# Optimization experiments

Hardware: AMD Instinct MI355X
Metric: run time of the kernel (lower is better)

The kernel has to match this reference:

```python
import jax, jax.numpy as jnp
import numpy as np

BETA = 0.25  # VectorQuantizer commitment beta


def setup_inputs() -> dict:
    key = jax.random.key(0)
    k1, k2, k3, k4 = jax.random.split(key, 4)
    B, T, Zc, D, K = 8, 4096, 512, 256, 8192
    x = jax.random.normal(k1, (B, T, 1, Zc), dtype=jnp.float32)
    W = jax.random.normal(k2, (Zc, D), dtype=jnp.float32) / np.sqrt(Zc)
    b = jax.random.normal(k3, (D,), dtype=jnp.float32) * 0.01
    codebook = jax.random.normal(k4, (K, D), dtype=jnp.float32) / np.sqrt(D)
    return {"x": x, "W": W, "b": b, "codebook": codebook}


def reference(x, W, b, codebook):
    sg = jax.lax.stop_gradient
    # quant_conv: Linear(z_channels -> embed_dim) after squeezing dim 2
    h = jnp.einsum('btc,cd->btd', jnp.squeeze(x, 2), W) + b  # [B,T,D]
    B, T, D = h.shape
    flat = h.reshape(-1, D)  # [B*T, D]
    # squared L2 distances to codebook: ||z||^2 + ||e||^2 - 2 z.e
    d = (jnp.sum(flat * flat, axis=1, keepdims=True)
         + jnp.sum(codebook * codebook, axis=1)
         - 2.0 * flat @ codebook.T)  # [B*T, K]
    idx = jnp.argmin(d, axis=1)  # [B*T]
    zq = jnp.take(codebook, idx, axis=0).reshape(B, T, D)
    # codebook + commitment loss
    emb_loss = (BETA * jnp.mean((sg(zq) - h) ** 2)
                + jnp.mean((zq - sg(h)) ** 2))
    # straight-through estimator
    zq = h + sg(zq - h)
    quant = zq[..., None]  # [B,T,D,1], matching h.unsqueeze(-1) layout
    return quant, emb_loss
```

## Files before the change

kernel.cpp:

```cpp
#include <hip/hip_runtime.h>
#include <stdint.h>

#define M_TOT 32768
#define ZC 512
#define DD 256
#define KCODES 8192
#define NGRAN 512
#define MARGIN 0.15f
#define NBUCKET 256

typedef _Float16 half8   __attribute__((ext_vector_type(8)));
typedef _Float16 half2v  __attribute__((ext_vector_type(2)));
typedef float    float4v __attribute__((ext_vector_type(4)));
typedef float    float16v __attribute__((ext_vector_type(16)));

#define OFF_H     0ull
#define OFF_HT    33554432ull
#define OFF_CBT   50331648ull
#define OFF_HH    54525952ull
#define OFF_EE    54657024ull
#define OFF_LOSSP 54689792ull
#define OFF_SMIN  54691840ull
#define OFF_WTH   OFF_SMIN
#define OFF_WTL   (OFF_SMIN + 524288ull)

#define ASYNC_CP16(gp, lp)                                                     \
  __builtin_amdgcn_global_load_lds(                                            \
      (const __attribute__((address_space(1))) void*)(gp),                     \
      (__attribute__((address_space(3))) void*)(lp), 16, 0, 0)

__global__ __launch_bounds__(256) void k_prep_w(const float* __restrict__ W,
                                                _Float16* __restrict__ wt_hi,
                                                _Float16* __restrict__ wt_lo) {
    const int idx = blockIdx.x * 256 + threadIdx.x;
    const int n = idx & 255, k = idx >> 8;
    const float v = W[(size_t)k * DD + n];
    const _Float16 hi = (_Float16)v;
    const _Float16 lo = (_Float16)(v - (float)hi);
    const int off = (((n >> 5) * 64 + (k >> 3)) << 8) + ((n & 31) << 3) + (k & 7);
    wt_hi[off] = hi;
    wt_lo[off] = lo;
}

__global__ __launch_bounds__(256) void k_gemm1(const float* __restrict__ x,
                                               const _Float16* __restrict__ wt_hi,
                                               const _Float16* __restrict__ wt_lo,
                                               const float* __restrict__ b,
                                               float* __restrict__ h) {
    __shared__ _Float16 sH[64 * 64];
    __shared__ _Float16 sL[64 * 64];
    const int tid = threadIdx.x, lane = tid & 63, w = tid >> 6;
    const int wy = w >> 1, wx = w & 1;
    const int m0 = blockIdx.x * 64;

    float16v acc[4];
#pragma unroll
    for (int j = 0; j < 4; ++j) acc[j] = (float16v)(0.0f);

    for (int kb = 0; kb < ZC; kb += 64) {
        __syncthreads();
        {
            const int m = tid & 63;
            const int kp = tid >> 6;
#pragma unroll
            for (int i2 = 0; i2 < 2; ++i2) {
                const int kg = kp * 2 + i2;
                const float* src = x + (size_t)(m0 + m) * ZC + kb + kg * 8;
                float4v v0 = *(const float4v*)src;
                float4v v1 = *(const float4v*)(src + 4);
                half8 hi, lo;
                float vv[8] = {v0.x, v0.y, v0.z, v0.w, v1.x, v1.y, v1.z, v1.w};
#pragma unroll
                for (int j = 0; j < 8; ++j) {
                    hi[j] = (_Float16)vv[j];
                    lo[j] = (_Float16)(vv[j] - (float)hi[j]);
                }
                const int off = (((m >> 5) * 8 + kg) << 8) + ((m & 31) << 3);
                *(half8*)&sH[off] = hi;
                *(half8*)&sL[off] = lo;
            }
        }
        __syncthreads();
#pragma unroll
        for (int s = 0; s < 4; ++s) {
            const int S = (kb >> 4) + s;
            half8 ah = *(const half8*)&sH[((wy * 8 + 2 * s) << 8) + lane * 8];
            half8 al = *(const half8*)&sL[((wy * 8 + 2 * s) << 8) + lane * 8];
#pragma unroll
            for (int nf = 0; nf < 4; ++nf) {
                const int nblk = wx * 4 + nf;
                const size_t boff = ((size_t)(nblk * 64 + 2 * S) << 8) + lane * 8;
                half8 bh = *(const half8*)&wt_hi[boff];
                half8 bl = *(const half8*)&wt_lo[boff];
                acc[nf] = __builtin_amdgcn_mfma_f32_32x32x16_f16(ah, bh, acc[nf], 0, 0, 0);
                acc[nf] = __builtin_amdgcn_mfma_f32_32x32x16_f16(ah, bl, acc[nf], 0, 0, 0);
                acc[nf] = __builtin_amdgcn_mfma_f32_32x32x16_f16(al, bh, acc[nf], 0, 0, 0);
            }
        }
    }
#pragma unroll
    for (int nf = 0; nf < 4; ++nf) {
        const int col = wx * 128 + nf * 32 + (lane & 31);
        const float bias = b[col];
#pragma unroll
        for (int r = 0; r < 16; ++r) {
            const int row = m0 + wy * 32 + (r & 3) + 8 * (r >> 2) + 4 * (lane >> 5);
            h[(size_t)row * DD + col] = acc[nf][r] + bias;
        }
    }
}

__global__ __launch_bounds__(256) void k_prep_h(const float* __restrict__ h,
                                                _Float16* __restrict__ ht,
                                                float* __restrict__ hh) {
    const int lane = threadIdx.x & 63, w = threadIdx.x >> 6;
    const int row = blockIdx.x * 4 + w;
    float4v v = *(const float4v*)&h[(size_t)row * DD + lane * 4];
    half2v p0, p1;
    p0.x = (_Float16)v.x; p0.y = (_Float16)v.y;
    p1.x = (_Float16)v.z; p1.y = (_Float16)v.w;
    const size_t off = ((size_t)((row >> 5) * 32 + (lane >> 1)) << 8) +
                       ((row & 31) << 3) + ((lane & 1) << 2);
    *(half2v*)&ht[off] = p0;
    *(half2v*)&ht[off + 2] = p1;
    float s = v.x * v.x + v.y * v.y + v.z * v.z + v.w * v.w;
#pragma unroll
    for (int o = 32; o; o >>= 1) s += __shfl_down(s, o);
    if (lane == 0) hh[row] = s;
}

__global__ __launch_bounds__(256) void k_prep_cb(const float* __restrict__ cb,
                                                 _Float16* __restrict__ cbt,
                                                 float* __restrict__ ee,
                                                 float* __restrict__ loss_part) {
    if (blockIdx.x == 0) loss_part[threadIdx.x] = 0.0f;
    const int lane = threadIdx.x & 63, w = threadIdx.x >> 6;
    const int code = blockIdx.x * 4 + w;
    float4v v = *(const float4v*)&cb[(size_t)code * DD + lane * 4];
    half2v p0, p1;
    p0.x = (_Float16)v.x; p0.y = (_Float16)v.y;
    p1.x = (_Float16)v.z; p1.y = (_Float16)v.w;
    const size_t off = ((size_t)((code >> 5) * 32 + (lane >> 1)) << 8) +
                       ((code & 31) << 3) + ((lane & 1) << 2);
    *(half2v*)&cbt[off] = p0;
    *(half2v*)&cbt[off + 2] = p1;
    float s = v.x * v.x + v.y * v.y + v.z * v.z + v.w * v.w;
#pragma unroll
    for (int o = 32; o; o >>= 1) s += __shfl_down(s, o);
    if (lane == 0) ee[code] = s;
}

__global__ __launch_bounds__(256, 2) void k_dist(const _Float16* __restrict__ ht,
                                                 const _Float16* __restrict__ cbt,
                                                 const float* __restrict__ ee,
                                                 _Float16* __restrict__ smin) {
    __shared__ _Float16 sB[2][64 * 256];
    const int tid = threadIdx.x, lane = tid & 63, w = tid >> 6;
    const int lw = lane & 31, csel = lane >> 5;
    const int bx = blockIdx.x;
    const int by = blockIdx.y;

    half8 afr[2][16];
    const size_t lo = (size_t)lane * 8;
#pragma unroll
    for (int mi = 0; mi < 2; ++mi) {
        const _Float16* base = cbt + (size_t)(bx * 8 + w * 2 + mi) * 8192;
#pragma unroll
        for (int s = 0; s < 16; ++s)
            afr[mi][s] = *(const half8*)(base + s * 512 + lo);
    }
    half8 aext[2], bext;
#pragma unroll
    for (int j = 0; j < 8; ++j) bext[j] = (_Float16)0.f;
    if (csel == 0) bext[0] = (_Float16)(-0.5f);
#pragma unroll
    for (int mi = 0; mi < 2; ++mi) {
        const float e = ee[bx * 256 + w * 64 + mi * 32 + lw];
#pragma unroll
        for (int j = 0; j < 8; ++j) aext[mi][j] = (_Float16)0.f;
        if (csel == 0) aext[mi][0] = (_Float16)e;
    }

    const _Float16* hbase = ht + (size_t)by * 1024 * 256 + (size_t)w * 4096 + lane * 8;
#define STAGE_HS(buf, t)                                                       \
    do {                                                                       \
        const _Float16* g_ = hbase + (size_t)(t) * 16384;                      \
        char* l_ = (char*)&sB[(buf)][0] + w * 8192;                            \
        _Pragma("unroll")                                                      \
        for (int i_ = 0; i_ < 8; ++i_)                                         \
            ASYNC_CP16(g_ + i_ * 512, l_ + i_ * 1024);                         \
    } while (0)

#define COMPUTE_HS(buf, t)                                                     \
    do {                                                                       \
        const int r0_ = by * 1024 + (t) * 64;                                  \
        const _Float16* sb_ = &sB[(buf)][0];                                   \
        _Pragma("unroll 1")                                                    \
        for (int nj = 0; nj < 2; ++nj) {                                       \
            float16v acc0 = (float16v)(0.f), acc1 = (float16v)(0.f);           \
            __builtin_amdgcn_s_setprio(1);                                     \
            _Pragma("unroll")                                                  \
            for (int s = 0; s < 16; ++s) {                                     \
                half8 bf = *(const half8*)&sb_[(size_t)((nj * 32 + 2 * s + csel) << 8) + lw * 8]; \
                acc0 = __builtin_amdgcn_mfma_f32_32x32x16_f16(afr[0][s], bf, acc0, 0, 0, 0); \
                acc1 = __builtin_amdgcn_mfma_f32_32x32x16_f16(afr[1][s], bf, acc1, 0, 0, 0); \
            }                                                                  \
            acc0 = __builtin_amdgcn_mfma_f32_32x32x16_f16(aext[0], bext, acc0, 0, 0, 0); \
            acc1 = __builtin_amdgcn_mfma_f32_32x32x16_f16(aext[1], bext, acc1, 0, 0, 0); \
            __builtin_amdgcn_s_setprio(0);                                     \
             \
             \
            float g0a = acc0[0], g1a = acc0[8];                                \
            float g0b = acc1[0], g1b = acc1[8];                                \
            _Pragma("unroll")                                                  \
            for (int r = 1; r < 8; ++r) {                                      \
                g0a = fmaxf(g0a, acc0[r]);  g1a = fmaxf(g1a, acc0[8 + r]);     \
                g0b = fmaxf(g0b, acc1[r]);  g1b = fmaxf(g1b, acc1[8 + r]);     \
            }                                                                  \
            g0a = fmaxf(g0a, __shfl_xor(g0a, 32));                             \
            g1a = fmaxf(g1a, __shfl_xor(g1a, 32));                             \
            g0b = fmaxf(g0b, __shfl_xor(g0b, 32));                             \
            g1b = fmaxf(g1b, __shfl_xor(g1b, 32));                             \
            if (lane < 32) {                                                   \
                const int row_ = r0_ + nj * 32 + lane;                         \
                const int gb_ = bx * 16 + w * 4;                               \
                smin[(size_t)(gb_ + 0) * M_TOT + row_] = (_Float16)(-2.f * g0a); \
                smin[(size_t)(gb_ + 1) * M_TOT + row_] = (_Float16)(-2.f * g1a); \
                smin[(size_t)(gb_ + 2) * M_TOT + row_] = (_Float16)(-2.f * g0b); \
                smin[(size_t)(gb_ + 3) * M_TOT + row_] = (_Float16)(-2.f * g1b); \
            }                                                                  \
        }                                                                      \
    } while (0)

    STAGE_HS(0, 0);

#pragma unroll 1
    for (int t = 0; t < 15; ++t) {
        const int cur = t & 1;
        STAGE_HS(cur ^ 1, t + 1);
        asm volatile("s_waitcnt vmcnt(8)" ::: "memory");
        __builtin_amdgcn_s_barrier();
        __builtin_amdgcn_sched_barrier(0);
        COMPUTE_HS(cur, t);
        __builtin_amdgcn_sched_barrier(0);
        __builtin_amdgcn_s_barrier();
    }
    asm volatile("s_waitcnt vmcnt(0)" ::: "memory");
    __builtin_amdgcn_s_barrier();
    __builtin_amdgcn_sched_barrier(0);
    COMPUTE_HS(1, 15);

#undef STAGE_HS
#undef COMPUTE_HS
}

__global__ __launch_bounds__(256, 2) void k_select(const float* __restrict__ h,
                                                   const float* __restrict__ cb,
                                                   const float* __restrict__ hh,
                                                   const float* __restrict__ ee,
                                                   const _Float16* __restrict__ smin,
                                                   float* __restrict__ out,
                                                   float* __restrict__ loss_part) {
    __shared__ _Float16 sS[64][512];
    const int t = threadIdx.x, lane = t & 63, w = t >> 6;
    const int r0 = blockIdx.x * 64;

    for (int gi = t; gi < NGRAN; gi += 256) {
        const _Float16* src = smin + (size_t)gi * M_TOT + r0;
#pragma unroll
        for (int c = 0; c < 8; ++c) {
            half8 v = *(const half8*)(src + c * 8);
#pragma unroll
            for (int j = 0; j < 8; ++j) sS[c * 8 + j][gi] = v[j];
        }
    }
    __syncthreads();

    float lossacc = 0.0f;
    for (int i = 0; i < 16; ++i) {
        const int row = r0 + w * 16 + i;
        float4v hv = *(const float4v*)&h[(size_t)row * DD + lane * 4];
        half8 sm = *(const half8*)&sS[w * 16 + i][lane * 8];
        float vmin = 1e30f;
        float sv[8];
#pragma unroll
        for (int j = 0; j < 8; ++j) {
            sv[j] = (float)sm[j];
            vmin = fminf(vmin, sv[j]);
        }
        float m2 = vmin;
#pragma unroll
        for (int o = 32; o; o >>= 1) m2 = fminf(m2, __shfl_xor(m2, o));
        const float thr = m2 + MARGIN;
        unsigned flags = 0;
#pragma unroll
        for (int j = 0; j < 8; ++j)
            if (sv[j] <= thr) flags |= (1u << j);

        unsigned long long act = __ballot(flags != 0);
        unsigned long long bestk = ~0ull;
        const float hhv = hh[row];
        while (act) {
            const int ln = __ffsll((long long)act) - 1;
            act &= act - 1;
            unsigned fl = (unsigned)__shfl((int)flags, ln);
            while (fl) {
                const int j = __ffs(fl) - 1;
                fl &= fl - 1;
                const int g = ln * 8 + j;
#pragma unroll
                for (int c = 0; c < 16; ++c) {
                    const int code = g * 16 + c;
                    float4v cv = *(const float4v*)&cb[(size_t)code * DD + lane * 4];
                    float s = hv.x * cv.x + hv.y * cv.y + hv.z * cv.z + hv.w * cv.w;
#pragma unroll
                    for (int o = 32; o; o >>= 1) s += __shfl_xor(s, o);
                    const float d = (hhv + ee[code]) - 2.0f * s;
                    const unsigned bts = __float_as_uint(d);
                    const unsigned mb =
                        bts ^ (unsigned)(((int)bts >> 31) | 0x80000000);
                    const unsigned long long key =
                        ((unsigned long long)mb << 32) | (unsigned)code;
                    if (key < bestk) bestk = key;
                }
            }
        }
        const unsigned best = (unsigned)(bestk & 0xffffffffull);
        float4v cv = *(const float4v*)&cb[(size_t)best * DD + lane * 4];
        *(float4v*)&out[(size_t)row * DD + lane * 4] = cv;
        const float dx = cv.x - hv.x, dy = cv.y - hv.y;
        const float dz = cv.z - hv.z, dw = cv.w - hv.w;
        lossacc += dx * dx + dy * dy + dz * dz + dw * dw;
    }
#pragma unroll
    for (int o = 32; o; o >>= 1) lossacc += __shfl_xor(lossacc, o);
    if (lane == 0)
        atomicAdd(&loss_part[(blockIdx.x * 4 + w) & (NBUCKET - 1)], lossacc);
}

__global__ __launch_bounds__(256) void k_final(const float* __restrict__ loss_part,
                                               float* __restrict__ out) {
    const int t = threadIdx.x;
    float s = loss_part[t];
#pragma unroll
    for (int off = 32; off; off >>= 1) s += __shfl_down(s, off);
    __shared__ float wsum[4];
    if ((t & 63) == 0) wsum[t >> 6] = s;
    __syncthreads();
    if (t == 0)
        out[0] = 1.25f * ((wsum[0] + wsum[1]) + (wsum[2] + wsum[3]))
                 / (float)(M_TOT * DD);
}

extern "C" void kernel_launch(void* const* d_in, const int* in_sizes, int n_in,
                              void* d_out, int out_size, void* d_ws, size_t ws_size,
                              hipStream_t stream) {
    const float* x  = (const float*)d_in[0];
    const float* W  = (const float*)d_in[1];
    const float* b  = (const float*)d_in[2];
    const float* cb = (const float*)d_in[3];
    float* out = (float*)d_out;

    char* ws = (char*)d_ws;
    float* h        = (float*)(ws + OFF_H);
    _Float16* ht    = (_Float16*)(ws + OFF_HT);
    _Float16* cbt   = (_Float16*)(ws + OFF_CBT);
    _Float16* wt_hi = (_Float16*)(ws + OFF_WTH);
    _Float16* wt_lo = (_Float16*)(ws + OFF_WTL);
    float* hh       = (float*)(ws + OFF_HH);
    float* ee       = (float*)(ws + OFF_EE);
    _Float16* smin  = (_Float16*)(ws + OFF_SMIN);
    float* loss_part = (float*)(ws + OFF_LOSSP);

    hipLaunchKernelGGL(k_prep_w, dim3(512), dim3(256), 0, stream, W, wt_hi, wt_lo);
    hipLaunchKernelGGL(k_prep_cb, dim3(KCODES / 4), dim3(256), 0, stream,
                       cb, cbt, ee, loss_part);
    hipLaunchKernelGGL(k_gemm1, dim3(M_TOT / 64), dim3(256), 0, stream,
                       x, wt_hi, wt_lo, b, h);
    hipLaunchKernelGGL(k_prep_h, dim3(M_TOT / 4), dim3(256), 0, stream,
                       h, ht, hh);
    hipLaunchKernelGGL(k_dist, dim3(KCODES / 256, M_TOT / 1024), dim3(256),
                       0, stream, ht, cbt, ee, smin);
    hipLaunchKernelGGL(k_select, dim3(M_TOT / 64), dim3(256), 0, stream,
                       h, cb, hh, ee, smin, out, loss_part);
    hipLaunchKernelGGL(k_final, dim3(1), dim3(256), 0, stream,
                       loss_part, out + (size_t)M_TOT * DD);
}
```

Before: 374.2 us.

## Software-pipeline LDS fragment reads with MFMA and relax vmcnt waits past stores

The distance-max kernel's inner compute now double-buffers B fragments in registers. The next four LDS reads are issued before the MFMAs that consume the current four, so LDS latency overlaps matrix work instead of serialising per step. The first tile is peeled, and the vmcnt waits are raised to count the outstanding smin global stores from the previous tile. The kernel then waits only for the staged loads and not for the stores. This uses more VGPRs for the fragment buffers, and correctness depends on the in-order vmcnt accounting staying exact.

```diff
diff --git a/kernel.cpp b/kernel.cpp
--- a/kernel.cpp
+++ b/kernel.cpp
@@ -191,67 +191,116 @@
             ASYNC_CP16(g_ + i_ * 512, l_ + i_ * 1024);                         \
     } while (0)
 
+#define LDB(sb_, nj_, s_)                                                      \
+    (*(const half8*)&(sb_)[(size_t)((((nj_) * 32) + 2 * (s_) + csel) << 8) + lw * 8])
+
+#define RD4(sb_, dst, nj_, s0)                                                 \
+    do {                                                                       \
+        dst[0] = LDB(sb_, nj_, (s0) + 0);                                      \
+        dst[1] = LDB(sb_, nj_, (s0) + 1);                                      \
+        dst[2] = LDB(sb_, nj_, (s0) + 2);                                      \
+        dst[3] = LDB(sb_, nj_, (s0) + 3);                                      \
+    } while (0)
+
+#define MM8(bfv, s0)                                                           \
+    do {                                                                       \
+        __builtin_amdgcn_s_setprio(1);                                         \
+        acc0 = __builtin_amdgcn_mfma_f32_32x32x16_f16(afr[0][(s0) + 0], bfv[0], acc0, 0, 0, 0); \
+        acc1 = __builtin_amdgcn_mfma_f32_32x32x16_f16(afr[1][(s0) + 0], bfv[0], acc1, 0, 0, 0); \
+        acc0 = __builtin_amdgcn_mfma_f32_32x32x16_f16(afr[0][(s0) + 1], bfv[1], acc0, 0, 0, 0); \
+        acc1 = __builtin_amdgcn_mfma_f32_32x32x16_f16(afr[1][(s0) + 1], bfv[1], acc1, 0, 0, 0); \
+        acc0 = __builtin_amdgcn_mfma_f32_32x32x16_f16(afr[0][(s0) + 2], bfv[2], acc0, 0, 0, 0); \
+        acc1 = __builtin_amdgcn_mfma_f32_32x32x16_f16(afr[1][(s0) + 2], bfv[2], acc1, 0, 0, 0); \
+        acc0 = __builtin_amdgcn_mfma_f32_32x32x16_f16(afr[0][(s0) + 3], bfv[3], acc0, 0, 0, 0); \
+        acc1 = __builtin_amdgcn_mfma_f32_32x32x16_f16(afr[1][(s0) + 3], bfv[3], acc1, 0, 0, 0); \
+        __builtin_amdgcn_s_setprio(0);                                         \
+    } while (0)
+
+#define MMEXT()                                                                \
+    do {                                                                       \
+        acc0 = __builtin_amdgcn_mfma_f32_32x32x16_f16(aext[0], bext, acc0, 0, 0, 0); \
+        acc1 = __builtin_amdgcn_mfma_f32_32x32x16_f16(aext[1], bext, acc1, 0, 0, 0); \
+    } while (0)
+
+#define EPI(nj_)                                                               \
+    do {                                                                       \
+        float g0a = acc0[0], g1a = acc0[8];                                    \
+        float g0b = acc1[0], g1b = acc1[8];                                    \
+        _Pragma("unroll")                                                      \
+        for (int r = 1; r < 8; ++r) {                                          \
+            g0a = fmaxf(g0a, acc0[r]);  g1a = fmaxf(g1a, acc0[8 + r]);         \
+            g0b = fmaxf(g0b, acc1[r]);  g1b = fmaxf(g1b, acc1[8 + r]);         \
+        }                                                                      \
+        g0a = fmaxf(g0a, __shfl_xor(g0a, 32));                                 \
+        g1a = fmaxf(g1a, __shfl_xor(g1a, 32));                                 \
+        g0b = fmaxf(g0b, __shfl_xor(g0b, 32));                                 \
+        g1b = fmaxf(g1b, __shfl_xor(g1b, 32));                                 \
+        if (lane < 32) {                                                       \
+            const int row_ = r0_ + (nj_) * 32 + lane;                          \
+            const int gb_ = bx * 16 + w * 4;                                   \
+            smin[(size_t)(gb_ + 0) * M_TOT + row_] = (_Float16)(-2.f * g0a);   \
+            smin[(size_t)(gb_ + 1) * M_TOT + row_] = (_Float16)(-2.f * g1a);   \
+            smin[(size_t)(gb_ + 2) * M_TOT + row_] = (_Float16)(-2.f * g0b);   \
+            smin[(size_t)(gb_ + 3) * M_TOT + row_] = (_Float16)(-2.f * g1b);   \
+        }                                                                      \
+    } while (0)
+
 #define COMPUTE_HS(buf, t)                                                     \
     do {                                                                       \
         const int r0_ = by * 1024 + (t) * 64;                                  \
         const _Float16* sb_ = &sB[(buf)][0];                                   \
-        _Pragma("unroll 1")                                                    \
-        for (int nj = 0; nj < 2; ++nj) {                                       \
-            float16v acc0 = (float16v)(0.f), acc1 = (float16v)(0.f);           \
-            __builtin_amdgcn_s_setprio(1);                                     \
-            _Pragma("unroll")                                                  \
-            for (int s = 0; s < 16; ++s) {                                     \
-                half8 bf = *(const half8*)&sb_[(size_t)((nj * 32 + 2 * s + csel) << 8) + lw * 8]; \
-                acc0 = __builtin_amdgcn_mfma_f32_32x32x16_f16(afr[0][s], bf, acc0, 0, 0, 0); \
-                acc1 = __builtin_amdgcn_mfma_f32_32x32x16_f16(afr[1][s], bf, acc1, 0, 0, 0); \
-            }                                                                  \
-            acc0 = __builtin_amdgcn_mfma_f32_32x32x16_f16(aext[0], bext, acc0, 0, 0, 0); \
-            acc1 = __builtin_amdgcn_mfma_f32_32x32x16_f16(aext[1], bext, acc1, 0, 0, 0); \
-            __builtin_amdgcn_s_setprio(0);                                     \
-             \
-             \
-            float g0a = acc0[0], g1a = acc0[8];                                \
-            float g0b = acc1[0], g1b = acc1[8];                                \
-            _Pragma("unroll")                                                  \
-            for (int r = 1; r < 8; ++r) {                                      \
-                g0a = fmaxf(g0a, acc0[r]);  g1a = fmaxf(g1a, acc0[8 + r]);     \
-                g0b = fmaxf(g0b, acc1[r]);  g1b = fmaxf(g1b, acc1[8 + r]);     \
-            }                                                                  \
-            g0a = fmaxf(g0a, __shfl_xor(g0a, 32));                             \
-            g1a = fmaxf(g1a, __shfl_xor(g1a, 32));                             \
-            g0b = fmaxf(g0b, __shfl_xor(g0b, 32));                             \
-            g1b = fmaxf(g1b, __shfl_xor(g1b, 32));                             \
-            if (lane < 32) {                                                   \
-                const int row_ = r0_ + nj * 32 + lane;                         \
-                const int gb_ = bx * 16 + w * 4;                               \
-                smin[(size_t)(gb_ + 0) * M_TOT + row_] = (_Float16)(-2.f * g0a); \
-                smin[(size_t)(gb_ + 1) * M_TOT + row_] = (_Float16)(-2.f * g1a); \
-                smin[(size_t)(gb_ + 2) * M_TOT + row_] = (_Float16)(-2.f * g0b); \
-                smin[(size_t)(gb_ + 3) * M_TOT + row_] = (_Float16)(-2.f * g1b); \
-            }                                                                  \
-        }                                                                      \
+        half8 bfA[4], bfB[4];                                                  \
+        float16v acc0 = (float16v)(0.f), acc1 = (float16v)(0.f);               \
+                                                                     \
+        RD4(sb_, bfA, 0, 0);                                                   \
+        RD4(sb_, bfB, 0, 4);   MM8(bfA, 0);                                    \
+        RD4(sb_, bfA, 0, 8);   MM8(bfB, 4);                                    \
+        RD4(sb_, bfB, 0, 12);  MM8(bfA, 8);                                    \
+        RD4(sb_, bfA, 1, 0);   MM8(bfB, 12);              \
+        MMEXT();                                                               \
+        EPI(0);                           \
+                                                                     \
+        acc0 = (float16v)(0.f); acc1 = (float16v)(0.f);                        \
+        RD4(sb_, bfB, 1, 4);   MM8(bfA, 0);                                    \
+        RD4(sb_, bfA, 1, 8);   MM8(bfB, 4);                                    \
+        RD4(sb_, bfB, 1, 12);  MM8(bfA, 8);                                    \
+        MM8(bfB, 12);                                                          \
+        MMEXT();                                                               \
+        EPI(1);                                                                \
     } while (0)
 
     STAGE_HS(0, 0);
+    STAGE_HS(1, 1);
+    asm volatile("s_waitcnt vmcnt(8)" ::: "memory");
+    __builtin_amdgcn_s_barrier();
+    __builtin_amdgcn_sched_barrier(0);
+    COMPUTE_HS(0, 0);
+    __builtin_amdgcn_sched_barrier(0);
+    __builtin_amdgcn_s_barrier();
 
 #pragma unroll 1
-    for (int t = 0; t < 15; ++t) {
+    for (int t = 1; t < 15; ++t) {
         const int cur = t & 1;
         STAGE_HS(cur ^ 1, t + 1);
-        asm volatile("s_waitcnt vmcnt(8)" ::: "memory");
+        asm volatile("s_waitcnt vmcnt(16)" ::: "memory");
         __builtin_amdgcn_s_barrier();
         __builtin_amdgcn_sched_barrier(0);
         COMPUTE_HS(cur, t);
         __builtin_amdgcn_sched_barrier(0);
         __builtin_amdgcn_s_barrier();
     }
-    asm volatile("s_waitcnt vmcnt(0)" ::: "memory");
+    asm volatile("s_waitcnt vmcnt(8)" ::: "memory");
     __builtin_amdgcn_s_barrier();
     __builtin_amdgcn_sched_barrier(0);
     COMPUTE_HS(1, 15);
 
 #undef STAGE_HS
 #undef COMPUTE_HS
+#undef LDB
+#undef RD4
+#undef MM8
+#undef MMEXT
+#undef EPI
 }
 
 __global__ __launch_bounds__(256, 2) void k_select(const float* __restrict__ h,
```

Result: no change. 370.4 us (-1.0%).
